# Optimization experiments

Hardware: AMD Instinct MI355X
Metric: run time of the kernel (lower is better)

The kernel has to match this reference:

```python
import jax, jax.numpy as jnp
import numpy as np

B, L, D = 2, 401, 128


def setup_inputs() -> dict:
    key = jax.random.key(0)
    ks = jax.random.split(key, 9)
    s = 1.0 / np.sqrt(D)
    return {
        "x": jax.random.normal(ks[0], (B, L, D), dtype=jnp.float32),
        # nn.Bilinear weight (out=D, in1=D, in2=D) and bias (D,)
        "W_bil": jax.random.uniform(ks[1], (D, D, D), jnp.float32, -s, s),
        "b_bil": jax.random.uniform(ks[2], (D,), jnp.float32, -s, s),
        # LayerNorm(D)
        "ln_g": jnp.ones((D,), jnp.float32),
        "ln_b": jnp.zeros((D,), jnp.float32),
        # Linear(D, D)
        "W1": jax.random.uniform(ks[3], (D, D), jnp.float32, -s, s),
        "b1": jax.random.uniform(ks[4], (D,), jnp.float32, -s, s),
        # Linear(D, 1)
        "w2": jax.random.uniform(ks[5], (D,), jnp.float32, -s, s),
        "b2": jax.random.uniform(ks[6], (1,), jnp.float32, -s, s),
    }


def reference(x, W_bil, b_bil, ln_g, ln_b, W1, b1, w2, b2):
    # Bilinear: pair[b,i,j,k] = x[b,i,:] @ W_bil[k] @ x[b,j,:] + b_bil[k]
    # Contract in two steps to avoid an O(L^2 D^2) intermediate:
    tmp = jnp.einsum('bid,kde->bike', x, W_bil)          # (B,L,D,D)
    pair = jnp.einsum('bike,bje->bijk', tmp, x) + b_bil  # (B,L,L,D)
    # LayerNorm over D
    mu = jnp.mean(pair, axis=-1, keepdims=True)
    var = jnp.mean(jnp.square(pair - mu), axis=-1, keepdims=True)
    h = (pair - mu) * jax.lax.rsqrt(var + 1e-5) * ln_g + ln_b
    # Linear -> GELU (exact, torch default) -> Dropout(eval: identity) -> Linear(D,1)
    h = jax.nn.gelu(jnp.einsum('bijd,ed->bije', h, W1) + b1, approximate=False)
    contact = jnp.einsum('bijd,d->bij', h, w2) + b2[0]   # (B,L,L)
    return 0.5 * (contact + jnp.swapaxes(contact, 1, 2))
```

## Files before the change

kernel.cpp:

```cpp
#include <hip/hip_runtime.h>
#include <hip/hip_bf16.h>

#define L 401
#define D 128
#define BATCH 2

typedef __attribute__((ext_vector_type(8))) short short8;
typedef __attribute__((ext_vector_type(4))) float f32x4;

__device__ __forceinline__ ushort bf16_bits(float f) {
  __hip_bfloat16 h = __float2bfloat16(f);
  return *reinterpret_cast<ushort*>(&h);
}

__device__ __forceinline__ short8 frag_read(const char* lds, int row, int cb) {
  return *(const short8*)(lds + row * 256 + (cb ^ ((row & 7) << 4)));
}

__device__ __forceinline__ void stage128x128(char* lds, const __hip_bfloat16* src,
                                             int row0, int rowmax, int tid) {
#pragma unroll
  for (int it = 0; it < 8; ++it) {
    int r = it * 16 + (tid >> 4);
    int cb = (tid & 15) * 16;
    int sr = row0 + r;
    sr = sr > rowmax ? rowmax : sr;
    short8 v = *(const short8*)((const char*)src + (size_t)sr * (D * 2) + cb);
    *(short8*)(lds + r * 256 + (cb ^ ((r & 7) << 4))) = v;
  }
}

__global__ void cast_kernel(const float* __restrict__ x, const float* __restrict__ w1,
                            __hip_bfloat16* __restrict__ xbf, __hip_bfloat16* __restrict__ w1bf) {
  int idx = blockIdx.x * 256 + threadIdx.x;
  const int n1 = BATCH * L * D;
  if (idx < n1) {
    xbf[idx] = __float2bfloat16(x[idx]);
  } else {
    int j = idx - n1;
    if (j < D * D) w1bf[j] = __float2bfloat16(w1[j]);
  }
}

__global__ void transpose_wbil(const float* __restrict__ Wb, __hip_bfloat16* __restrict__ wbt) {
  int k = blockIdx.x;
  const float* in = Wb + (size_t)k * D * D;
  __hip_bfloat16* out = wbt + (size_t)k * D * D;
  for (int n = threadIdx.x; n < (D / 4) * D; n += 256) {
    int d0 = (n >> 7) * 4;
    int e = n & 127;
    ushort4 o;
    o.x = bf16_bits(in[(d0 + 0) * D + e]);
    o.y = bf16_bits(in[(d0 + 1) * D + e]);
    o.z = bf16_bits(in[(d0 + 2) * D + e]);
    o.w = bf16_bits(in[(d0 + 3) * D + e]);
    *(ushort4*)((ushort*)out + e * D + d0) = o;
  }
}

__global__ __launch_bounds__(256, 2) void gemm_tmp(const __hip_bfloat16* __restrict__ xbf,
                                                   const __hip_bfloat16* __restrict__ wbt,
                                                   __hip_bfloat16* __restrict__ tmp) {
  __shared__ char ldsA[128 * 256];
  __shared__ char ldsB[128 * 256];
  const int tid = threadIdx.x;
  const int lane = tid & 63;
  const int w = tid >> 6;
  const int c0 = lane & 15;
  const int lg = lane >> 4;
  const int kt = blockIdx.x;
  const int i0 = blockIdx.y * 128;
  const int b = blockIdx.z;

  stage128x128(ldsA, xbf + (size_t)b * L * D, i0, L - 1, tid);
  stage128x128(ldsB, wbt + (size_t)kt * D * D, 0, 127, tid);
  __syncthreads();

  f32x4 acc[2][8];
#pragma unroll
  for (int rf = 0; rf < 2; ++rf)
#pragma unroll
    for (int cf = 0; cf < 8; ++cf) acc[rf][cf] = (f32x4){0.f, 0.f, 0.f, 0.f};

#pragma unroll
  for (int ks = 0; ks < 4; ++ks) {
    const int cb = ks * 64 + lg * 16;
    short8 a0 = frag_read(ldsA, w * 32 + c0, cb);
    short8 a1 = frag_read(ldsA, w * 32 + 16 + c0, cb);
#pragma unroll
    for (int cf = 0; cf < 8; ++cf) {
      short8 bb = frag_read(ldsB, cf * 16 + c0, cb);
      acc[0][cf] = __builtin_amdgcn_mfma_f32_16x16x32_bf16(a0, bb, acc[0][cf], 0, 0, 0);
      acc[1][cf] = __builtin_amdgcn_mfma_f32_16x16x32_bf16(a1, bb, acc[1][cf], 0, 0, 0);
    }
  }

  ushort* out = (ushort*)tmp;
#pragma unroll
  for (int rf = 0; rf < 2; ++rf)
#pragma unroll
    for (int cf = 0; cf < 8; ++cf)
#pragma unroll
      for (int r = 0; r < 4; ++r) {
        int i = i0 + w * 32 + rf * 16 + lg * 4 + r;
        if (i < L) {
          int col = cf * 16 + c0;
          out[((size_t)(b * L + i)) * (D * D) + kt * D + col] = bf16_bits(acc[rf][cf][r]);
        }
      }
}

__global__ __launch_bounds__(256, 2) void fused_contact(
    const __hip_bfloat16* __restrict__ xbf, const __hip_bfloat16* __restrict__ tmp,
    const __hip_bfloat16* __restrict__ w1bf, const float* __restrict__ b_bil,
    const float* __restrict__ ln_g, const float* __restrict__ ln_b,
    const float* __restrict__ b1, const float* __restrict__ w2,
    const float* __restrict__ b2, float* __restrict__ cont) {
  __shared__ char ldsX[128 * 256];
  __shared__ char ldsT[128 * 256];
  const int tid = threadIdx.x;
  const int lane = tid & 63;
  const int w = tid >> 6;
  const int c0 = lane & 15;
  const int lg = lane >> 4;
  const int b = blockIdx.z;
  const int i = blockIdx.y;
  const int j0 = blockIdx.x * 128;

  stage128x128(ldsX, xbf + (size_t)b * L * D, j0, L - 1, tid);
  stage128x128(ldsT, tmp + ((size_t)(b * L + i)) * (D * D), 0, 127, tid);
  __syncthreads();

  f32x4 acc[2][8];
#pragma unroll
  for (int rf = 0; rf < 2; ++rf)
#pragma unroll
    for (int cf = 0; cf < 8; ++cf) acc[rf][cf] = (f32x4){0.f, 0.f, 0.f, 0.f};

#pragma unroll
  for (int ks = 0; ks < 4; ++ks) {
    const int cb = ks * 64 + lg * 16;
    short8 a0 = frag_read(ldsX, w * 32 + c0, cb);
    short8 a1 = frag_read(ldsX, w * 32 + 16 + c0, cb);
#pragma unroll
    for (int cf = 0; cf < 8; ++cf) {
      short8 bb = frag_read(ldsT, cf * 16 + c0, cb);
      acc[0][cf] = __builtin_amdgcn_mfma_f32_16x16x32_bf16(a0, bb, acc[0][cf], 0, 0, 0);
      acc[1][cf] = __builtin_amdgcn_mfma_f32_16x16x32_bf16(a1, bb, acc[1][cf], 0, 0, 0);
    }
  }

  float lngv[8], lnbv[8];
#pragma unroll
  for (int cf = 0; cf < 8; ++cf) {
    const int c = cf * 16 + c0;
    const float bbia = b_bil[c];
#pragma unroll
    for (int rf = 0; rf < 2; ++rf)
#pragma unroll
      for (int r = 0; r < 4; ++r) acc[rf][cf][r] += bbia;
    lngv[cf] = ln_g[c];
    lnbv[cf] = ln_b[c];
  }
  float mu[2][4], rs[2][4];
#pragma unroll
  for (int rf = 0; rf < 2; ++rf)
#pragma unroll
    for (int r = 0; r < 4; ++r) {
      float s = 0.f, q = 0.f;
#pragma unroll
      for (int cf = 0; cf < 8; ++cf) {
        float v = acc[rf][cf][r];
        s += v;
        q += v * v;
      }
      s += __shfl_xor(s, 1); s += __shfl_xor(s, 2); s += __shfl_xor(s, 4); s += __shfl_xor(s, 8);
      q += __shfl_xor(q, 1); q += __shfl_xor(q, 2); q += __shfl_xor(q, 4); q += __shfl_xor(q, 8);
      const float m = s * (1.f / 128.f);
      float var = q * (1.f / 128.f) - m * m;
      mu[rf][r] = m;
      rs[rf][r] = rsqrtf(var + 1e-5f);
    }

  __syncthreads();

#pragma unroll
  for (int rf = 0; rf < 2; ++rf)
#pragma unroll
    for (int cf = 0; cf < 8; ++cf)
#pragma unroll
      for (int r = 0; r < 4; ++r) {
        const int row = w * 32 + rf * 16 + lg * 4 + r;
        const int colb = (cf * 16 + c0) * 2;
        const float v = (acc[rf][cf][r] - mu[rf][r]) * rs[rf][r] * lngv[cf] + lnbv[cf];
        *(ushort*)(ldsX + row * 256 + (colb ^ ((row & 7) << 4))) = bf16_bits(v);
      }
  stage128x128(ldsT, w1bf, 0, 127, tid);
  __syncthreads();

  f32x4 acc2[2][8];
#pragma unroll
  for (int rf = 0; rf < 2; ++rf)
#pragma unroll
    for (int cf = 0; cf < 8; ++cf) acc2[rf][cf] = (f32x4){0.f, 0.f, 0.f, 0.f};

#pragma unroll
  for (int ks = 0; ks < 4; ++ks) {
    const int cb = ks * 64 + lg * 16;
    short8 a0 = frag_read(ldsX, w * 32 + c0, cb);
    short8 a1 = frag_read(ldsX, w * 32 + 16 + c0, cb);
#pragma unroll
    for (int cf = 0; cf < 8; ++cf) {
      short8 bb = frag_read(ldsT, cf * 16 + c0, cb);
      acc2[0][cf] = __builtin_amdgcn_mfma_f32_16x16x32_bf16(a0, bb, acc2[0][cf], 0, 0, 0);
      acc2[1][cf] = __builtin_amdgcn_mfma_f32_16x16x32_bf16(a1, bb, acc2[1][cf], 0, 0, 0);
    }
  }

  float b1v[8], w2v[8];
#pragma unroll
  for (int cf = 0; cf < 8; ++cf) {
    const int c = cf * 16 + c0;
    b1v[cf] = b1[c];
    w2v[cf] = w2[c];
  }
  const float b2v = b2[0];
  float part[2][4];
#pragma unroll
  for (int rf = 0; rf < 2; ++rf)
#pragma unroll
    for (int r = 0; r < 4; ++r) part[rf][r] = 0.f;
#pragma unroll
  for (int rf = 0; rf < 2; ++rf)
#pragma unroll
    for (int cf = 0; cf < 8; ++cf)
#pragma unroll
      for (int r = 0; r < 4; ++r) {
        const float v = acc2[rf][cf][r] + b1v[cf];
        const float g = 0.5f * v * (1.f + erff(v * 0.70710678118654752f));
        part[rf][r] += g * w2v[cf];
      }
#pragma unroll
  for (int rf = 0; rf < 2; ++rf)
#pragma unroll
    for (int r = 0; r < 4; ++r) {
      float p = part[rf][r];
      p += __shfl_xor(p, 1); p += __shfl_xor(p, 2); p += __shfl_xor(p, 4); p += __shfl_xor(p, 8);
      if (c0 == 0) {
        const int j = j0 + w * 32 + rf * 16 + lg * 4 + r;
        if (j < L) cont[((size_t)(b * L + i)) * L + j] = p + b2v;
      }
    }
}

__global__ void sym_kernel(const float* __restrict__ c, float* __restrict__ out) {
  int idx = blockIdx.x * 256 + threadIdx.x;
  const int n = BATCH * L * L;
  if (idx >= n) return;
  int b = idx / (L * L);
  int r = idx - b * (L * L);
  int i = r / L;
  int j = r - i * L;
  out[idx] = 0.5f * (c[(size_t)b * L * L + (size_t)i * L + j] +
                     c[(size_t)b * L * L + (size_t)j * L + i]);
}

extern "C" void kernel_launch(void* const* d_in, const int* in_sizes, int n_in,
                              void* d_out, int out_size, void* d_ws, size_t ws_size,
                              hipStream_t stream) {
  const float* x     = (const float*)d_in[0];
  const float* W_bil = (const float*)d_in[1];
  const float* b_bil = (const float*)d_in[2];
  const float* ln_g  = (const float*)d_in[3];
  const float* ln_b  = (const float*)d_in[4];
  const float* W1    = (const float*)d_in[5];
  const float* b1    = (const float*)d_in[6];
  const float* w2    = (const float*)d_in[7];
  const float* b2    = (const float*)d_in[8];
  float* out = (float*)d_out;

  char* ws = (char*)d_ws;
  __hip_bfloat16* xbf  = (__hip_bfloat16*)(ws + 0);
  __hip_bfloat16* w1bf = (__hip_bfloat16*)(ws + 205312);
  __hip_bfloat16* wbt  = (__hip_bfloat16*)(ws + 238080);
  __hip_bfloat16* tmp  = (__hip_bfloat16*)(ws + 4432384);
  float* cont          = (float*)(ws + 30712320);

  const int ncast = BATCH * L * D + D * D;
  cast_kernel<<<(ncast + 255) / 256, 256, 0, stream>>>(x, W1, xbf, w1bf);
  transpose_wbil<<<D, 256, 0, stream>>>(W_bil, wbt);
  gemm_tmp<<<dim3(D, 4, BATCH), 256, 0, stream>>>(xbf, wbt, tmp);
  fused_contact<<<dim3(4, L, BATCH), 256, 0, stream>>>(xbf, tmp, w1bf, b_bil, ln_g, ln_b,
                                                       b1, w2, b2, cont);
  sym_kernel<<<(BATCH * L * L + 255) / 256, 256, 0, stream>>>(cont, out);
}
```

Before: 199.5 us.

## Use 512-thread blocks, fast GELU, LDS-tiled Wbil transpose, vectorized tmp stores

Both GEMM kernels move to 512-thread blocks where each wave owns 16 rows instead of 32, halving per-thread accumulators so occupancy can rise. gemm_tmp swaps operand roles so each lane holds four consecutive e outputs, which lets it write tmp with 8-byte packed stores instead of scattered 2-byte ones. The erf-based GELU becomes a polynomial approximation built on hardware rcp and exp2, and rsqrt uses the raw hardware instruction. transpose_wbil now reads coalesced float4 and transposes through LDS. Together these cut register pressure, store traffic and transcendental cost, at the price of a small accuracy loss in GELU.

```diff
diff --git a/kernel.cpp b/kernel.cpp
--- a/kernel.cpp
+++ b/kernel.cpp
@@ -17,17 +17,31 @@
   return *(const short8*)(lds + row * 256 + (cb ^ ((row & 7) << 4)));
 }
 
-__device__ __forceinline__ void stage128x128(char* lds, const __hip_bfloat16* src,
-                                             int row0, int rowmax, int tid) {
-#pragma unroll
-  for (int it = 0; it < 8; ++it) {
-    int r = it * 16 + (tid >> 4);
+__device__ __forceinline__ void stage128x128_512(char* lds, const __hip_bfloat16* src,
+                                                 int row0, int rowmax, int tid) {
+#pragma unroll
+  for (int it = 0; it < 4; ++it) {
+    int r = it * 32 + (tid >> 4);
     int cb = (tid & 15) * 16;
     int sr = row0 + r;
     sr = sr > rowmax ? rowmax : sr;
     short8 v = *(const short8*)((const char*)src + (size_t)sr * (D * 2) + cb);
     *(short8*)(lds + r * 256 + (cb ^ ((r & 7) << 4))) = v;
   }
+}
+
+__device__ __forceinline__ float gelu_fast(float v) {
+  const float a = fabsf(v) * 0.70710678118654752f;
+  const float t = __builtin_amdgcn_rcpf(fmaf(a, 0.3275911f, 1.0f));
+  float p = fmaf(t, 0.530702714f, -0.726576013f);
+  p = fmaf(p, t, 0.710706870f);
+  p = fmaf(p, t, -0.142248368f);
+  p = fmaf(p, t, 0.127414796f);
+  p = p * t;
+  const float e = __builtin_amdgcn_exp2f(a * a * -1.4426950408889634f);
+  const float q = p * e;
+  const float cdf = (v < 0.f) ? q : 1.0f - q;
+  return v * cdf;
 }
 
 __global__ void cast_kernel(const float* __restrict__ x, const float* __restrict__ w1,
@@ -43,26 +57,36 @@
 }
 
 __global__ void transpose_wbil(const float* __restrict__ Wb, __hip_bfloat16* __restrict__ wbt) {
-  int k = blockIdx.x;
+  __shared__ alignas(16) ushort t[128 * 136];
+  const int tid = threadIdx.x;
+  const int k = blockIdx.x;
   const float* in = Wb + (size_t)k * D * D;
-  __hip_bfloat16* out = wbt + (size_t)k * D * D;
-  for (int n = threadIdx.x; n < (D / 4) * D; n += 256) {
-    int d0 = (n >> 7) * 4;
-    int e = n & 127;
-    ushort4 o;
-    o.x = bf16_bits(in[(d0 + 0) * D + e]);
-    o.y = bf16_bits(in[(d0 + 1) * D + e]);
-    o.z = bf16_bits(in[(d0 + 2) * D + e]);
-    o.w = bf16_bits(in[(d0 + 3) * D + e]);
-    *(ushort4*)((ushort*)out + e * D + d0) = o;
-  }
-}
-
-__global__ __launch_bounds__(256, 2) void gemm_tmp(const __hip_bfloat16* __restrict__ xbf,
+#pragma unroll
+  for (int it = 0; it < 16; ++it) {
+    int idx = it * 256 + tid;
+    int d = idx >> 5;
+    int e = (idx & 31) * 4;
+    float4 f4 = ((const float4*)in)[idx];
+    t[(e + 0) * 136 + d] = bf16_bits(f4.x);
+    t[(e + 1) * 136 + d] = bf16_bits(f4.y);
+    t[(e + 2) * 136 + d] = bf16_bits(f4.z);
+    t[(e + 3) * 136 + d] = bf16_bits(f4.w);
+  }
+  __syncthreads();
+  ushort* out = (ushort*)(wbt + (size_t)k * D * D);
+  const int e = tid >> 1;
+  const int d0 = (tid & 1) * 64;
+#pragma unroll
+  for (int c = 0; c < 16; ++c) {
+    *(ushort4*)&out[e * D + d0 + c * 4] = *(ushort4*)&t[e * 136 + d0 + c * 4];
+  }
+}
+
+__global__ __launch_bounds__(512, 4) void gemm_tmp(const __hip_bfloat16* __restrict__ xbf,
                                                    const __hip_bfloat16* __restrict__ wbt,
                                                    __hip_bfloat16* __restrict__ tmp) {
-  __shared__ char ldsA[128 * 256];
-  __shared__ char ldsB[128 * 256];
+  __shared__ char ldsE[128 * 256];
+  __shared__ char ldsI[128 * 256];
   const int tid = threadIdx.x;
   const int lane = tid & 63;
   const int w = tid >> 6;
@@ -72,45 +96,40 @@
   const int i0 = blockIdx.y * 128;
   const int b = blockIdx.z;
 
-  stage128x128(ldsA, xbf + (size_t)b * L * D, i0, L - 1, tid);
-  stage128x128(ldsB, wbt + (size_t)kt * D * D, 0, 127, tid);
-  __syncthreads();
-
-  f32x4 acc[2][8];
-#pragma unroll
-  for (int rf = 0; rf < 2; ++rf)
-#pragma unroll
-    for (int cf = 0; cf < 8; ++cf) acc[rf][cf] = (f32x4){0.f, 0.f, 0.f, 0.f};
+  stage128x128_512(ldsI, xbf + (size_t)b * L * D, i0, L - 1, tid);
+  stage128x128_512(ldsE, wbt + (size_t)kt * D * D, 0, 127, tid);
+  __syncthreads();
+
+  f32x4 acc[8];
+#pragma unroll
+  for (int cf = 0; cf < 8; ++cf) acc[cf] = (f32x4){0.f, 0.f, 0.f, 0.f};
 
 #pragma unroll
   for (int ks = 0; ks < 4; ++ks) {
     const int cb = ks * 64 + lg * 16;
-    short8 a0 = frag_read(ldsA, w * 32 + c0, cb);
-    short8 a1 = frag_read(ldsA, w * 32 + 16 + c0, cb);
-#pragma unroll
-    for (int cf = 0; cf < 8; ++cf) {
-      short8 bb = frag_read(ldsB, cf * 16 + c0, cb);
-      acc[0][cf] = __builtin_amdgcn_mfma_f32_16x16x32_bf16(a0, bb, acc[0][cf], 0, 0, 0);
-      acc[1][cf] = __builtin_amdgcn_mfma_f32_16x16x32_bf16(a1, bb, acc[1][cf], 0, 0, 0);
-    }
-  }
-
-  ushort* out = (ushort*)tmp;
-#pragma unroll
-  for (int rf = 0; rf < 2; ++rf)
-#pragma unroll
-    for (int cf = 0; cf < 8; ++cf)
-#pragma unroll
-      for (int r = 0; r < 4; ++r) {
-        int i = i0 + w * 32 + rf * 16 + lg * 4 + r;
-        if (i < L) {
-          int col = cf * 16 + c0;
-          out[((size_t)(b * L + i)) * (D * D) + kt * D + col] = bf16_bits(acc[rf][cf][r]);
-        }
-      }
-}
-
-__global__ __launch_bounds__(256, 2) void fused_contact(
+    short8 ae = frag_read(ldsE, w * 16 + c0, cb);
+#pragma unroll
+    for (int cf = 0; cf < 8; ++cf) {
+      short8 bi = frag_read(ldsI, cf * 16 + c0, cb);
+      acc[cf] = __builtin_amdgcn_mfma_f32_16x16x32_bf16(ae, bi, acc[cf], 0, 0, 0);
+    }
+  }
+
+  ushort* outp = (ushort*)tmp;
+  const int e0 = w * 16 + lg * 4;
+#pragma unroll
+  for (int cf = 0; cf < 8; ++cf) {
+    const int i = i0 + cf * 16 + c0;
+    if (i < L) {
+      uint lo = (uint)bf16_bits(acc[cf][0]) | ((uint)bf16_bits(acc[cf][1]) << 16);
+      uint hi = (uint)bf16_bits(acc[cf][2]) | ((uint)bf16_bits(acc[cf][3]) << 16);
+      uint2 v; v.x = lo; v.y = hi;
+      *(uint2*)(outp + ((size_t)(b * L + i)) * (D * D) + kt * D + e0) = v;
+    }
+  }
+}
+
+__global__ __launch_bounds__(512, 4) void fused_contact(
     const __hip_bfloat16* __restrict__ xbf, const __hip_bfloat16* __restrict__ tmp,
     const __hip_bfloat16* __restrict__ w1bf, const float* __restrict__ b_bil,
     const float* __restrict__ ln_g, const float* __restrict__ ln_b,
@@ -127,26 +146,22 @@
   const int i = blockIdx.y;
   const int j0 = blockIdx.x * 128;
 
-  stage128x128(ldsX, xbf + (size_t)b * L * D, j0, L - 1, tid);
-  stage128x128(ldsT, tmp + ((size_t)(b * L + i)) * (D * D), 0, 127, tid);
-  __syncthreads();
-
-  f32x4 acc[2][8];
-#pragma unroll
-  for (int rf = 0; rf < 2; ++rf)
-#pragma unroll
-    for (int cf = 0; cf < 8; ++cf) acc[rf][cf] = (f32x4){0.f, 0.f, 0.f, 0.f};
+  stage128x128_512(ldsX, xbf + (size_t)b * L * D, j0, L - 1, tid);
+  stage128x128_512(ldsT, tmp + ((size_t)(b * L + i)) * (D * D), 0, 127, tid);
+  __syncthreads();
+
+  f32x4 acc[8];
+#pragma unroll
+  for (int cf = 0; cf < 8; ++cf) acc[cf] = (f32x4){0.f, 0.f, 0.f, 0.f};
 
 #pragma unroll
   for (int ks = 0; ks < 4; ++ks) {
     const int cb = ks * 64 + lg * 16;
-    short8 a0 = frag_read(ldsX, w * 32 + c0, cb);
-    short8 a1 = frag_read(ldsX, w * 32 + 16 + c0, cb);
+    short8 a0 = frag_read(ldsX, w * 16 + c0, cb);
 #pragma unroll
     for (int cf = 0; cf < 8; ++cf) {
       short8 bb = frag_read(ldsT, cf * 16 + c0, cb);
-      acc[0][cf] = __builtin_amdgcn_mfma_f32_16x16x32_bf16(a0, bb, acc[0][cf], 0, 0, 0);
-      acc[1][cf] = __builtin_amdgcn_mfma_f32_16x16x32_bf16(a1, bb, acc[1][cf], 0, 0, 0);
+      acc[cf] = __builtin_amdgcn_mfma_f32_16x16x32_bf16(a0, bb, acc[cf], 0, 0, 0);
     }
   }
 
@@ -156,64 +171,54 @@
     const int c = cf * 16 + c0;
     const float bbia = b_bil[c];
 #pragma unroll
-    for (int rf = 0; rf < 2; ++rf)
-#pragma unroll
-      for (int r = 0; r < 4; ++r) acc[rf][cf][r] += bbia;
+    for (int r = 0; r < 4; ++r) acc[cf][r] += bbia;
     lngv[cf] = ln_g[c];
     lnbv[cf] = ln_b[c];
   }
-  float mu[2][4], rs[2][4];
-#pragma unroll
-  for (int rf = 0; rf < 2; ++rf)
+  float mu[4], rs[4];
+#pragma unroll
+  for (int r = 0; r < 4; ++r) {
+    float s = 0.f, q = 0.f;
+#pragma unroll
+    for (int cf = 0; cf < 8; ++cf) {
+      float v = acc[cf][r];
+      s += v;
+      q += v * v;
+    }
+    s += __shfl_xor(s, 1); s += __shfl_xor(s, 2); s += __shfl_xor(s, 4); s += __shfl_xor(s, 8);
+    q += __shfl_xor(q, 1); q += __shfl_xor(q, 2); q += __shfl_xor(q, 4); q += __shfl_xor(q, 8);
+    const float m = s * (1.f / 128.f);
+    float var = q * (1.f / 128.f) - m * m;
+    mu[r] = m;
+    rs[r] = __builtin_amdgcn_rsqf(var + 1e-5f);
+  }
+
+  __syncthreads();
+
+#pragma unroll
+  for (int cf = 0; cf < 8; ++cf)
 #pragma unroll
     for (int r = 0; r < 4; ++r) {
-      float s = 0.f, q = 0.f;
-#pragma unroll
-      for (int cf = 0; cf < 8; ++cf) {
-        float v = acc[rf][cf][r];
-        s += v;
-        q += v * v;
-      }
-      s += __shfl_xor(s, 1); s += __shfl_xor(s, 2); s += __shfl_xor(s, 4); s += __shfl_xor(s, 8);
-      q += __shfl_xor(q, 1); q += __shfl_xor(q, 2); q += __shfl_xor(q, 4); q += __shfl_xor(q, 8);
-      const float m = s * (1.f / 128.f);
-      float var = q * (1.f / 128.f) - m * m;
-      mu[rf][r] = m;
-      rs[rf][r] = rsqrtf(var + 1e-5f);
-    }
-
-  __syncthreads();
-
-#pragma unroll
-  for (int rf = 0; rf < 2; ++rf)
-#pragma unroll
-    for (int cf = 0; cf < 8; ++cf)
-#pragma unroll
-      for (int r = 0; r < 4; ++r) {
-        const int row = w * 32 + rf * 16 + lg * 4 + r;
-        const int colb = (cf * 16 + c0) * 2;
-        const float v = (acc[rf][cf][r] - mu[rf][r]) * rs[rf][r] * lngv[cf] + lnbv[cf];
-        *(ushort*)(ldsX + row * 256 + (colb ^ ((row & 7) << 4))) = bf16_bits(v);
-      }
-  stage128x128(ldsT, w1bf, 0, 127, tid);
-  __syncthreads();
-
-  f32x4 acc2[2][8];
-#pragma unroll
-  for (int rf = 0; rf < 2; ++rf)
-#pragma unroll
-    for (int cf = 0; cf < 8; ++cf) acc2[rf][cf] = (f32x4){0.f, 0.f, 0.f, 0.f};
+      const int row = w * 16 + lg * 4 + r;
+      const int colb = (cf * 16 + c0) * 2;
+      const float v = (acc[cf][r] - mu[r]) * rs[r] * lngv[cf] + lnbv[cf];
+      *(ushort*)(ldsX + row * 256 + (colb ^ ((row & 7) << 4))) = bf16_bits(v);
+    }
+  stage128x128_512(ldsT, w1bf, 0, 127, tid);
+  __syncthreads();
+
+  f32x4 acc2[8];
+#pragma unroll
+  for (int cf = 0; cf < 8; ++cf) acc2[cf] = (f32x4){0.f, 0.f, 0.f, 0.f};
 
 #pragma unroll
   for (int ks = 0; ks < 4; ++ks) {
     const int cb = ks * 64 + lg * 16;
-    short8 a0 = frag_read(ldsX, w * 32 + c0, cb);
-    short8 a1 = frag_read(ldsX, w * 32 + 16 + c0, cb);
+    short8 a0 = frag_read(ldsX, w * 16 + c0, cb);
 #pragma unroll
     for (int cf = 0; cf < 8; ++cf) {
       short8 bb = frag_read(ldsT, cf * 16 + c0, cb);
-      acc2[0][cf] = __builtin_amdgcn_mfma_f32_16x16x32_bf16(a0, bb, acc2[0][cf], 0, 0, 0);
-      acc2[1][cf] = __builtin_amdgcn_mfma_f32_16x16x32_bf16(a1, bb, acc2[1][cf], 0, 0, 0);
+      acc2[cf] = __builtin_amdgcn_mfma_f32_16x16x32_bf16(a0, bb, acc2[cf], 0, 0, 0);
     }
   }
 
@@ -225,32 +230,23 @@
     w2v[cf] = w2[c];
   }
   const float b2v = b2[0];
-  float part[2][4];
-#pragma unroll
-  for (int rf = 0; rf < 2; ++rf)
-#pragma unroll
-    for (int r = 0; r < 4; ++r) part[rf][r] = 0.f;
-#pragma unroll
-  for (int rf = 0; rf < 2; ++rf)
-#pragma unroll
-    for (int cf = 0; cf < 8; ++cf)
-#pragma unroll
-      for (int r = 0; r < 4; ++r) {
-        const float v = acc2[rf][cf][r] + b1v[cf];
-        const float g = 0.5f * v * (1.f + erff(v * 0.70710678118654752f));
-        part[rf][r] += g * w2v[cf];
-      }
-#pragma unroll
-  for (int rf = 0; rf < 2; ++rf)
+  float part[4] = {0.f, 0.f, 0.f, 0.f};
+#pragma unroll
+  for (int cf = 0; cf < 8; ++cf)
 #pragma unroll
     for (int r = 0; r < 4; ++r) {
-      float p = part[rf][r];
-      p += __shfl_xor(p, 1); p += __shfl_xor(p, 2); p += __shfl_xor(p, 4); p += __shfl_xor(p, 8);
-      if (c0 == 0) {
-        const int j = j0 + w * 32 + rf * 16 + lg * 4 + r;
-        if (j < L) cont[((size_t)(b * L + i)) * L + j] = p + b2v;
-      }
-    }
+      const float v = acc2[cf][r] + b1v[cf];
+      part[r] += gelu_fast(v) * w2v[cf];
+    }
+#pragma unroll
+  for (int r = 0; r < 4; ++r) {
+    float p = part[r];
+    p += __shfl_xor(p, 1); p += __shfl_xor(p, 2); p += __shfl_xor(p, 4); p += __shfl_xor(p, 8);
+    if (c0 == 0) {
+      const int j = j0 + w * 16 + lg * 4 + r;
+      if (j < L) cont[((size_t)(b * L + i)) * L + j] = p + b2v;
+    }
+  }
 }
 
 __global__ void sym_kernel(const float* __restrict__ c, float* __restrict__ out) {
@@ -289,8 +285,8 @@
   const int ncast = BATCH * L * D + D * D;
   cast_kernel<<<(ncast + 255) / 256, 256, 0, stream>>>(x, W1, xbf, w1bf);
   transpose_wbil<<<D, 256, 0, stream>>>(W_bil, wbt);
-  gemm_tmp<<<dim3(D, 4, BATCH), 256, 0, stream>>>(xbf, wbt, tmp);
-  fused_contact<<<dim3(4, L, BATCH), 256, 0, stream>>>(xbf, tmp, w1bf, b_bil, ln_g, ln_b,
+  gemm_tmp<<<dim3(D, 4, BATCH), 512, 0, stream>>>(xbf, wbt, tmp);
+  fused_contact<<<dim3(4, L, BATCH), 512, 0, stream>>>(xbf, tmp, w1bf, b_bil, ln_g, ln_b,
                                                        b1, w2, b2, cont);
   sym_kernel<<<(BATCH * L * L + 255) / 256, 256, 0, stream>>>(cont, out);
 }
```

Measured after the change: 169.3 us. 1.18x faster.
